# Kernel optimization log

Measured on AMD Instinct MI355X. Metric: run time of the kernel, lower is better.

The kernel has to match this reference:

```python
import jax, jax.numpy as jnp
import numpy as np

N_NODES = 10000
N_EDGES = 160000
ATOMIC_DIM = 16          # C: multiplicity of 0e input irreps
L_VALUES = [0, 1, 2]
EDGE_DIM = 16            # number of bessel basis functions
HIDDEN_DIM = 16          # H: multiplicity of each output irrep
RADIUS_CUTOFF = 6.0
DEGREE_NORM = 16.0
SILU_GAIN = 1.679177     # e3nn normalize2mom gain for silu
WEIGHT_NUMEL = len(L_VALUES) * ATOMIC_DIM * HIDDEN_DIM  # 768


def bessel_basis(dist, num_basis, cutoff):
    # e3nn soft_one_hot_linspace, basis='bessel', start=0, cutoff=True
    x = dist[:, None]                                   # [E,1]
    n = jnp.arange(1, num_basis + 1, dtype=dist.dtype) * jnp.pi
    x_safe = jnp.where(x > 0, x, 1.0)
    out = jnp.sqrt(2.0 / cutoff) * jnp.sin(n * x / cutoff) / x_safe
    out = out * ((x < cutoff) & (x > 0))
    return out * jnp.sqrt(float(num_basis))             # EdgeEmbedding scaling


def spherical_harmonics(u):
    # e3nn real spherical harmonics l=0,1,2, 'component' convention, then
    # 'integral' normalization (divide by sqrt(4*pi)). u: unit vectors [E,3].
    x, y, z = u[:, 0], u[:, 1], u[:, 2]
    s3, s5, s15 = jnp.sqrt(3.0), jnp.sqrt(5.0), jnp.sqrt(15.0)
    y0 = jnp.ones_like(x)[:, None]
    y1 = jnp.stack([s3 * x, s3 * y, s3 * z], axis=-1)
    y2 = jnp.stack([
        s15 * x * z,
        s15 * x * y,
        s5 * (y * y - 0.5 * (x * x + z * z)),
        s15 * y * z,
        0.5 * s15 * (z * z - x * x),
    ], axis=-1)
    Y = jnp.concatenate([y0, y1, y2], axis=-1)          # [E, 9]
    return Y / jnp.sqrt(4.0 * jnp.pi)


def setup_inputs() -> dict:
    key = jax.random.key(0)
    k1, k2, k3, k4, k5 = jax.random.split(key, 5)
    atomic_features = jax.random.normal(k1, (N_NODES, ATOMIC_DIM), dtype=jnp.float32)
    coords = jax.random.normal(k2, (N_NODES, 3), dtype=jnp.float32) * 3.0
    edge_index = jax.random.randint(k3, (2, N_EDGES), 0, N_NODES, dtype=jnp.int64)
    W1 = jax.random.normal(k4, (EDGE_DIM, HIDDEN_DIM), dtype=jnp.float32)
    W2 = jax.random.normal(k5, (HIDDEN_DIM, WEIGHT_NUMEL), dtype=jnp.float32)
    return {"atomic_features": atomic_features, "coords": coords,
            "edge_index": edge_index, "W1": W1, "W2": W2}


def reference(atomic_features, coords, edge_index, W1, W2):
    src, dst = edge_index[0], edge_index[1]
    rel = coords[src] - coords[dst]                     # [E,3]
    dist = jnp.linalg.norm(rel, axis=-1)                # [E]
    # 1. spherical harmonic projection of normalized edge vectors
    u = rel / jnp.maximum(dist, 1e-12)[:, None]
    Y = spherical_harmonics(u)                          # [E,9]
    # 2. radial bessel basis
    eb = bessel_basis(dist, EDGE_DIM, RADIUS_CUTOFF)    # [E,edge_dim]
    # 3. FC net (e3nn FullyConnectedNet: /sqrt(fan_in), normalized silu)
    h = SILU_GAIN * jax.nn.silu(eb @ W1 / jnp.sqrt(float(EDGE_DIM)))
    edge_z = h @ W2 / jnp.sqrt(float(HIDDEN_DIM))       # [E, weight_numel]
    # 4. fully-connected tensor product Cx0e x (1x0e+1x1o+1x2e) -> Hx(...)
    E = edge_z.shape[0]
    w = edge_z.reshape(E, len(L_VALUES), ATOMIC_DIM, HIDDEN_DIM)
    xs = atomic_features[src]                           # [E,C]
    inv_sqrt_c = 1.0 / jnp.sqrt(float(ATOMIC_DIM))      # e3nn path normalization
    outs, off = [], 0
    for i, l in enumerate(L_VALUES):
        d = 2 * l + 1
        Yl = Y[:, off:off + d]                          # [E,d]
        m = jnp.einsum('ec,em,ech->ehm', xs, Yl, w[:, i]) * inv_sqrt_c
        outs.append(m.reshape(E, HIDDEN_DIM * d))
        off += d
    messages = jnp.concatenate(outs, axis=-1)           # [E, H*9]
    # 5. scatter-aggregate by destination node, degree normalization
    hidden = jax.ops.segment_sum(messages, dst, num_segments=N_NODES)
    return hidden / DEGREE_NORM
```

## Files before the change

kernel.cpp:

```cpp
#include <hip/hip_runtime.h>
#include <math.h>


typedef __attribute__((ext_vector_type(8))) short short8;
typedef __attribute__((ext_vector_type(4))) float f32x4;

static __device__ __forceinline__ unsigned short f2bf(float f) {
  unsigned u = __builtin_bit_cast(unsigned, f);
  u = (u + 0x7FFFu + ((u >> 16) & 1u)) >> 16;
  return (unsigned short)u;
}
static __device__ __forceinline__ float bf2f(unsigned short s) {
  unsigned u = ((unsigned)s) << 16;
  return __builtin_bit_cast(float, u);
}

__global__ void w2f_build(const float* __restrict__ W2, unsigned short* __restrict__ w2f) {
  int gid = blockIdx.x * 256 + threadIdx.x;
  if (gid >= 24 * 64) return;
  int fi = gid >> 6, lane = gid & 63;
  int s = fi / 3, t = fi - 3 * s;
  int h = lane & 15, kq = lane >> 4;
  short8 pack;
  #pragma unroll
  for (int j = 0; j < 8; ++j) {
    int kg = s * 32 + kq * 8 + j;
    int kk = kg >> 4, c = kg & 15;
    pack[j] = (short)f2bf(W2[kk * 768 + t * 256 + c * 16 + h]);
  }
  *(short8*)&w2f[(size_t)gid * 8] = pack;
}

__global__ __launch_bounds__(256, 2)
void interact_kernel(const float* __restrict__ xfeat,
                     const float* __restrict__ coords,
                     const int* __restrict__ eidx,
                     const float* __restrict__ W1g,
                     const unsigned short* __restrict__ w2f,
                     unsigned short* __restrict__ data,
                     int* __restrict__ head,
                     int* __restrict__ next,
                     int E)
{
  __shared__ float W1s[256];
  __shared__ float hsS[256 * 20];
  __shared__ __align__(16) unsigned short xsS[256 * 24];
  __shared__ int eS[256];
  __shared__ int wsum[4];

  const int tid  = threadIdx.x;
  const int lane = tid & 63, wid = tid >> 6;
  W1s[tid] = W1g[tid];

  const int e = blockIdx.x * 256 + tid;
  bool act = false;
  int src = 0, dst = 0;
  float rx = 0.f, ry = 0.f, rz = 0.f, d2 = 0.f;
  if (e < E) {
    src = eidx[e]; dst = eidx[E + e];
    rx = coords[3*src]   - coords[3*dst];
    ry = coords[3*src+1] - coords[3*dst+1];
    rz = coords[3*src+2] - coords[3*dst+2];
    d2 = rx*rx + ry*ry + rz*rz;
    act = (d2 > 0.0f) && (d2 < 36.0f);
  }
  unsigned long long bm = __ballot(act);
  int pfx = __popcll(bm & ((1ull << lane) - 1ull));
  if (lane == 0) wsum[wid] = __popcll(bm);
  __syncthreads();
  int base = 0;
  #pragma unroll
  for (int w = 0; w < 4; ++w) base += (w < wid) ? wsum[w] : 0;
  const int total = wsum[0] + wsum[1] + wsum[2] + wsum[3];
  const int cpos = base + pfx;

  if (act) {
    float dd  = sqrtf(d2);
    float inv = 1.0f / dd;
    float x = rx*inv, y = ry*inv, z = rz*inv;
    const float A0 = 0.28209479177387814f;
    const float A1 = 0.48860251190291992f;
    const float A2 = 1.09254843059207907f;
    const float A3 = 0.63078313050504001f;
    unsigned short* dr = data + (size_t)e * 64;
    dr[48] = f2bf(A0);
    dr[49] = f2bf(A1*x);   dr[50] = f2bf(A1*y);   dr[51] = f2bf(A1*z);
    dr[52] = f2bf(A2*x*z); dr[53] = f2bf(A2*x*y);
    dr[54] = f2bf(A3*(y*y - 0.5f*(x*x + z*z)));
    dr[55] = f2bf(A2*y*z);
    dr[56] = f2bf(0.5f*A2*(z*z - x*x));
    next[e] = atomicExch(&head[dst], e);

    float theta = 0.52359877559829887f * dd;
    float s1 = __sinf(theta), c1 = __cosf(theta);
    float snm = 0.0f, sn = s1;
    float hb[16];
    #pragma unroll
    for (int j = 0; j < 16; ++j) hb[j] = 0.0f;
    #pragma unroll
    for (int k = 0; k < 16; ++k) {
      #pragma unroll
      for (int j = 0; j < 16; ++j) hb[j] = fmaf(sn, W1s[k*16 + j], hb[j]);
      float sp = 2.0f*c1*sn - snm;
      snm = sn; sn = sp;
    }
    const float scale1 = 2.30940107675850305f * inv * 0.25f;
    float* hrow = &hsS[cpos * 20];
    #pragma unroll
    for (int j = 0; j < 16; ++j) {
      float p = hb[j] * scale1;
      hrow[j] = 1.679177f * p / (1.0f + __expf(-p));
    }
    unsigned short* xrow = &xsS[cpos * 24];
    #pragma unroll
    for (int cc = 0; cc < 4; ++cc) {
      float4 xv = *(const float4*)&xfeat[src*16 + cc*4];
      xrow[cc*4+0] = f2bf(xv.x); xrow[cc*4+1] = f2bf(xv.y);
      xrow[cc*4+2] = f2bf(xv.z); xrow[cc*4+3] = f2bf(xv.w);
    }
    eS[cpos] = e;
  }
  const int padded = (total + 15) & ~15;
  if (tid >= total && tid < padded) {
    #pragma unroll
    for (int j = 0; j < 16; ++j) hsS[tid*20 + j] = 0.0f;
    #pragma unroll
    for (int j = 0; j < 16; ++j) xsS[tid*24 + j] = 0;
  }
  __syncthreads();

  short8 bfr[8][3];
  #pragma unroll
  for (int s = 0; s < 8; ++s)
    #pragma unroll
    for (int t = 0; t < 3; ++t)
      bfr[s][t] = *(const short8*)&w2f[(size_t)((s*3 + t)*64 + lane) * 8];

  const int ngroups = padded >> 4;
  const int ma = lane & 15, kq = lane >> 4;
  const int c0 = (kq & 1) * 8;
  for (int g = wid; g < ngroups; g += 4) {
    const int cidx = g*16 + ma;
    const float* hrow = &hsS[cidx * 20];
    const unsigned short* xrow = &xsS[cidx * 24];
    float xsf[8];
    #pragma unroll
    for (int j = 0; j < 8; ++j) xsf[j] = bf2f(xrow[c0 + j]);

    f32x4 acc0 = {0,0,0,0}, acc1 = {0,0,0,0}, acc2 = {0,0,0,0};
    #pragma unroll
    for (int s = 0; s < 8; ++s) {
      const float hk = hrow[2*s + (kq >> 1)];
      short8 a;
      #pragma unroll
      for (int j = 0; j < 8; ++j) a[j] = (short)f2bf(hk * xsf[j]);
      acc0 = __builtin_amdgcn_mfma_f32_16x16x32_bf16(a, bfr[s][0], acc0, 0, 0, 0);
      acc1 = __builtin_amdgcn_mfma_f32_16x16x32_bf16(a, bfr[s][1], acc1, 0, 0, 0);
      acc2 = __builtin_amdgcn_mfma_f32_16x16x32_bf16(a, bfr[s][2], acc2, 0, 0, 0);
    }
    const float sc = 0.00390625f;
    #pragma unroll
    for (int r = 0; r < 4; ++r) {
      const int cr = g*16 + kq*4 + r;
      if (cr < total) {
        unsigned short* dr = data + (size_t)eS[cr] * 64;
        dr[ 0 + ma] = f2bf(acc0[r] * sc);
        dr[16 + ma] = f2bf(acc1[r] * sc);
        dr[32 + ma] = f2bf(acc2[r] * sc);
      }
    }
  }
}

__global__ __launch_bounds__(256)
void gather_kernel(const unsigned short* __restrict__ data,
                   const int* __restrict__ head,
                   const int* __restrict__ next,
                   float* __restrict__ out, int N)
{
  int gid = blockIdx.x * 256 + threadIdx.x;
  int node = gid >> 4, h = gid & 15;
  if (node >= N) return;

  float a0 = 0.f;
  float a10 = 0.f, a11 = 0.f, a12 = 0.f;
  float a20 = 0.f, a21 = 0.f, a22 = 0.f, a23 = 0.f, a24 = 0.f;

  int p = head[node];
  while (p >= 0) {
    const unsigned short* dr = data + (size_t)p * 64;
    float v0 = bf2f(dr[h]), v1 = bf2f(dr[16 + h]), v2 = bf2f(dr[32 + h]);
    a0  = fmaf(v0, bf2f(dr[48]), a0);
    a10 = fmaf(v1, bf2f(dr[49]), a10);
    a11 = fmaf(v1, bf2f(dr[50]), a11);
    a12 = fmaf(v1, bf2f(dr[51]), a12);
    a20 = fmaf(v2, bf2f(dr[52]), a20);
    a21 = fmaf(v2, bf2f(dr[53]), a21);
    a22 = fmaf(v2, bf2f(dr[54]), a22);
    a23 = fmaf(v2, bf2f(dr[55]), a23);
    a24 = fmaf(v2, bf2f(dr[56]), a24);
    p = next[p];
  }

  float* o = out + (size_t)node * 144;
  o[h] = a0;
  o[16 + h*3 + 0] = a10;
  o[16 + h*3 + 1] = a11;
  o[16 + h*3 + 2] = a12;
  o[64 + h*5 + 0] = a20;
  o[64 + h*5 + 1] = a21;
  o[64 + h*5 + 2] = a22;
  o[64 + h*5 + 3] = a23;
  o[64 + h*5 + 4] = a24;
}

extern "C" void kernel_launch(void* const* d_in, const int* in_sizes, int n_in,
                              void* d_out, int out_size, void* d_ws, size_t ws_size,
                              hipStream_t stream) {
  const float* xfeat  = (const float*)d_in[0];
  const float* coords = (const float*)d_in[1];
  const int*   eidx   = (const int*)d_in[2];
  const float* W1     = (const float*)d_in[3];
  const float* W2     = (const float*)d_in[4];
  float* out = (float*)d_out;

  const int E = in_sizes[2] / 2;
  const int N = out_size / 144;

  char* ws = (char*)d_ws;
  size_t off_head = (size_t)E * 64 * sizeof(unsigned short);
  size_t off_next = off_head + (size_t)N * sizeof(int);
  size_t off_w2f  = off_next + (size_t)E * sizeof(int);
  unsigned short* data = (unsigned short*)ws;
  int* head = (int*)(ws + off_head);
  int* next = (int*)(ws + off_next);
  unsigned short* w2f = (unsigned short*)(ws + off_w2f);

  hipMemsetAsync(head, 0xFF, (size_t)N * sizeof(int), stream);

  w2f_build<<<6, 256, 0, stream>>>(W2, w2f);
  interact_kernel<<<(E + 255) / 256, 256, 0, stream>>>(xfeat, coords, eidx, W1,
                                                       w2f, data, head, next, E);
  gather_kernel<<<(N * 16 + 255) / 256, 256, 0, stream>>>(data, head, next, out, N);
}
```

Before: 38.21 us.

## Interleave per-edge message layout, vectorize stores/loads, fuse head init into prep kernel

Changes the per-edge workspace record to a 72-element stride that interleaves the three l-channel values per hidden index and packs the eight non-constant spherical harmonics into one 16-byte vector. The interact kernel and the gather kernel now use vector stores and loads, and the constant Y0 factor is applied once at output instead of being stored per edge. The head memset is folded into the W2 packing kernel to save a launch, and the occupancy hint on interact_kernel is raised to 3 blocks per SM. In exchange the per-edge record grows, and the stricter occupancy bound may force register spills.

```diff
diff --git a/kernel.cpp b/kernel.cpp
--- a/kernel.cpp
+++ b/kernel.cpp
@@ -4,6 +4,9 @@
 
 typedef __attribute__((ext_vector_type(8))) short short8;
 typedef __attribute__((ext_vector_type(4))) float f32x4;
+typedef __attribute__((ext_vector_type(4))) unsigned short u16x4;
+
+#define DSTRIDE 72
 
 static __device__ __forceinline__ unsigned short f2bf(float f) {
   unsigned u = __builtin_bit_cast(unsigned, f);
@@ -15,23 +18,27 @@
   return __builtin_bit_cast(float, u);
 }
 
-__global__ void w2f_build(const float* __restrict__ W2, unsigned short* __restrict__ w2f) {
+__global__ __launch_bounds__(256)
+void prep_kernel(const float* __restrict__ W2, unsigned short* __restrict__ w2f,
+                 int* __restrict__ head, int N) {
   int gid = blockIdx.x * 256 + threadIdx.x;
-  if (gid >= 24 * 64) return;
-  int fi = gid >> 6, lane = gid & 63;
-  int s = fi / 3, t = fi - 3 * s;
-  int h = lane & 15, kq = lane >> 4;
-  short8 pack;
-  #pragma unroll
-  for (int j = 0; j < 8; ++j) {
-    int kg = s * 32 + kq * 8 + j;
-    int kk = kg >> 4, c = kg & 15;
-    pack[j] = (short)f2bf(W2[kk * 768 + t * 256 + c * 16 + h]);
-  }
-  *(short8*)&w2f[(size_t)gid * 8] = pack;
-}
-
-__global__ __launch_bounds__(256, 2)
+  if (gid < N) head[gid] = -1;
+  if (gid < 24 * 64) {
+    int fi = gid >> 6, lane = gid & 63;
+    int s = fi / 3, t = fi - 3 * s;
+    int h = lane & 15, kq = lane >> 4;
+    short8 pack;
+    #pragma unroll
+    for (int j = 0; j < 8; ++j) {
+      int kg = s * 32 + kq * 8 + j;
+      int kk = kg >> 4, c = kg & 15;
+      pack[j] = (short)f2bf(W2[kk * 768 + t * 256 + c * 16 + h]);
+    }
+    *(short8*)&w2f[(size_t)gid * 8] = pack;
+  }
+}
+
+__global__ __launch_bounds__(256, 3)
 void interact_kernel(const float* __restrict__ xfeat,
                      const float* __restrict__ coords,
                      const int* __restrict__ eidx,
@@ -78,17 +85,16 @@
     float dd  = sqrtf(d2);
     float inv = 1.0f / dd;
     float x = rx*inv, y = ry*inv, z = rz*inv;
-    const float A0 = 0.28209479177387814f;
     const float A1 = 0.48860251190291992f;
     const float A2 = 1.09254843059207907f;
     const float A3 = 0.63078313050504001f;
-    unsigned short* dr = data + (size_t)e * 64;
-    dr[48] = f2bf(A0);
-    dr[49] = f2bf(A1*x);   dr[50] = f2bf(A1*y);   dr[51] = f2bf(A1*z);
-    dr[52] = f2bf(A2*x*z); dr[53] = f2bf(A2*x*y);
-    dr[54] = f2bf(A3*(y*y - 0.5f*(x*x + z*z)));
-    dr[55] = f2bf(A2*y*z);
-    dr[56] = f2bf(0.5f*A2*(z*z - x*x));
+    unsigned short* dr = data + (size_t)e * DSTRIDE;
+    short8 ys;
+    ys[0] = (short)f2bf(A1*x);   ys[1] = (short)f2bf(A1*y);  ys[2] = (short)f2bf(A1*z);
+    ys[3] = (short)f2bf(A2*x*z); ys[4] = (short)f2bf(A2*x*y);
+    ys[5] = (short)f2bf(A3*(y*y - 0.5f*(x*x + z*z)));
+    ys[6] = (short)f2bf(A2*y*z); ys[7] = (short)f2bf(0.5f*A2*(z*z - x*x));
+    *(short8*)&dr[64] = ys;
     next[e] = atomicExch(&head[dst], e);
 
     float theta = 0.52359877559829887f * dd;
@@ -163,10 +169,13 @@
     for (int r = 0; r < 4; ++r) {
       const int cr = g*16 + kq*4 + r;
       if (cr < total) {
-        unsigned short* dr = data + (size_t)eS[cr] * 64;
-        dr[ 0 + ma] = f2bf(acc0[r] * sc);
-        dr[16 + ma] = f2bf(acc1[r] * sc);
-        dr[32 + ma] = f2bf(acc2[r] * sc);
+        unsigned short* dr = data + (size_t)eS[cr] * DSTRIDE;
+        u16x4 vv;
+        vv[0] = f2bf(acc0[r] * sc);
+        vv[1] = f2bf(acc1[r] * sc);
+        vv[2] = f2bf(acc2[r] * sc);
+        vv[3] = 0;
+        *(u16x4*)&dr[ma * 4] = vv;
       }
     }
   }
@@ -188,22 +197,25 @@
 
   int p = head[node];
   while (p >= 0) {
-    const unsigned short* dr = data + (size_t)p * 64;
-    float v0 = bf2f(dr[h]), v1 = bf2f(dr[16 + h]), v2 = bf2f(dr[32 + h]);
-    a0  = fmaf(v0, bf2f(dr[48]), a0);
-    a10 = fmaf(v1, bf2f(dr[49]), a10);
-    a11 = fmaf(v1, bf2f(dr[50]), a11);
-    a12 = fmaf(v1, bf2f(dr[51]), a12);
-    a20 = fmaf(v2, bf2f(dr[52]), a20);
-    a21 = fmaf(v2, bf2f(dr[53]), a21);
-    a22 = fmaf(v2, bf2f(dr[54]), a22);
-    a23 = fmaf(v2, bf2f(dr[55]), a23);
-    a24 = fmaf(v2, bf2f(dr[56]), a24);
-    p = next[p];
+    const unsigned short* dr = data + (size_t)p * DSTRIDE;
+    int pn = next[p];
+    u16x4 vv = *(const u16x4*)&dr[h * 4];
+    short8 yv = *(const short8*)&dr[64];
+    float v0 = bf2f(vv[0]), v1 = bf2f(vv[1]), v2 = bf2f(vv[2]);
+    a0  += v0;
+    a10 = fmaf(v1, bf2f((unsigned short)yv[0]), a10);
+    a11 = fmaf(v1, bf2f((unsigned short)yv[1]), a11);
+    a12 = fmaf(v1, bf2f((unsigned short)yv[2]), a12);
+    a20 = fmaf(v2, bf2f((unsigned short)yv[3]), a20);
+    a21 = fmaf(v2, bf2f((unsigned short)yv[4]), a21);
+    a22 = fmaf(v2, bf2f((unsigned short)yv[5]), a22);
+    a23 = fmaf(v2, bf2f((unsigned short)yv[6]), a23);
+    a24 = fmaf(v2, bf2f((unsigned short)yv[7]), a24);
+    p = pn;
   }
 
   float* o = out + (size_t)node * 144;
-  o[h] = a0;
+  o[h] = a0 * 0.28209479177387814f;
   o[16 + h*3 + 0] = a10;
   o[16 + h*3 + 1] = a11;
   o[16 + h*3 + 2] = a12;
@@ -228,17 +240,17 @@
   const int N = out_size / 144;
 
   char* ws = (char*)d_ws;
-  size_t off_head = (size_t)E * 64 * sizeof(unsigned short);
-  size_t off_next = off_head + (size_t)N * sizeof(int);
+  size_t off_head = (size_t)E * DSTRIDE * sizeof(unsigned short);
+  size_t off_next = off_head + (size_t)((N + 3) & ~3) * sizeof(int);
   size_t off_w2f  = off_next + (size_t)E * sizeof(int);
   unsigned short* data = (unsigned short*)ws;
   int* head = (int*)(ws + off_head);
   int* next = (int*)(ws + off_next);
   unsigned short* w2f = (unsigned short*)(ws + off_w2f);
 
-  hipMemsetAsync(head, 0xFF, (size_t)N * sizeof(int), stream);
-
-  w2f_build<<<6, 256, 0, stream>>>(W2, w2f);
+  int pblk = (N + 255) / 256;
+  if (pblk < 6) pblk = 6;
+  prep_kernel<<<pblk, 256, 0, stream>>>(W2, w2f, head, N);
   interact_kernel<<<(E + 255) / 256, 256, 0, stream>>>(xfeat, coords, eidx, W1,
                                                        w2f, data, head, next, E);
   gather_kernel<<<(N * 16 + 255) / 256, 256, 0, stream>>>(data, head, next, out, N);
```

New measurement: 37.44 us. -2.0%, faster.
